# Kernel optimization log

Measured on AMD Instinct MI355X. Metric: run time of the kernel, lower is better.

## Reference

```python
import jax, jax.numpy as jnp
import numpy as np


def setup_inputs() -> dict:
    key = jax.random.key(0)
    k1, k2 = jax.random.split(key)
    B, K, S = 262144, 32, 30
    sparse_code = jax.random.normal(k1, (B, K), dtype=jnp.float32)
    dictionary = jax.random.normal(k2, (S * S, K), dtype=jnp.float32)
    return {"sparse_code": sparse_code, "dictionary": dictionary, "image_size": S}


def reference(sparse_code, dictionary, image_size):
    # matmul(dictionary, sparse_code.T).T == sparse_code @ dictionary.T -> [B, S*S]
    samples = jnp.einsum("bk,dk->bd", sparse_code, dictionary)
    B = samples.shape[0]
    img = samples.reshape(B, image_size, image_size)
    # Serpentine unrolling: flip every odd row (rows 1,3,...,image_size-1)
    img = img.at[:, 1::2, :].set(img[:, 1::2, ::-1])
    return img[:, None, :, :]  # [B, 1, S, S]
```

## Files before the change

### kernel.cpp

```cpp
#include <hip/hip_runtime.h>
#include <hip/hip_bf16.h>


typedef __attribute__((ext_vector_type(8))) short bf16x8;
typedef __attribute__((ext_vector_type(4))) float f32x4;

constexpr int KD    = 32;
constexpr int DDIM  = 900;
constexpr int SDIM  = 30;
constexpr int NCHT  = 57;
constexpr int TROWS = 16;
constexpr int TILES = 8;
constexpr int RPB   = TROWS * TILES;

__device__ __forceinline__ int serp_src(int d) {
    int r = d / SDIM, c = d - r * SDIM;
    return (r & 1) ? (r * SDIM + (SDIM - 1 - c)) : d;
}

__device__ __forceinline__ short f2bf(float x) {
    __hip_bfloat16 h = __float2bfloat16(x);
    short u; __builtin_memcpy(&u, &h, 2); return u;
}

__device__ __forceinline__ void barrier_lds() {
    __builtin_amdgcn_sched_barrier(0);
    asm volatile("s_waitcnt lgkmcnt(0)" ::: "memory");
    __builtin_amdgcn_sched_barrier(0);
    __builtin_amdgcn_s_barrier();
    __builtin_amdgcn_sched_barrier(0);
}

__global__ __launch_bounds__(256) void mfma_decode(
    const float* __restrict__ sc,
    const float* __restrict__ dict,
    float* __restrict__ out,
    int B)
{
    __shared__ alignas(16) float stg[TROWS * DDIM];

    const int t    = threadIdx.x;
    const int lane = t & 63;
    const int wid  = t >> 6;

    bf16x8 df[15];
    #pragma unroll
    for (int j = 0; j < 15; ++j) {
        int ch = wid + 4 * j; if (ch > NCHT - 1) ch = NCHT - 1;
        int d  = ch * 16 + (lane & 15);
        int dd = (d < DDIM) ? d : (DDIM - 1);
        const float* p = dict + (size_t)serp_src(dd) * KD + ((lane >> 4) << 3);
        const float4 f0 = *reinterpret_cast<const float4*>(p);
        const float4 f1 = *reinterpret_cast<const float4*>(p + 4);
        bf16x8 a;
        a[0] = f2bf(f0.x); a[1] = f2bf(f0.y); a[2] = f2bf(f0.z); a[3] = f2bf(f0.w);
        a[4] = f2bf(f1.x); a[5] = f2bf(f1.y); a[6] = f2bf(f1.z); a[7] = f2bf(f1.w);
        df[j] = a;
    }

    const int brow = lane & 15;
    const int k0   = (lane >> 4) << 3;
    const int dloc = (lane >> 4) << 2;
    const long long b0 = (long long)blockIdx.x * RPB;

    const float* ap0 = sc + (size_t)(b0 + brow) * KD + k0;
    float4 pf0 = *reinterpret_cast<const float4*>(ap0);
    float4 pf1 = *reinterpret_cast<const float4*>(ap0 + 4);

    for (int tile = 0; tile < TILES; ++tile) {
        const long long rowg = b0 + (long long)tile * TROWS;

        bf16x8 bb;
        bb[0] = f2bf(pf0.x); bb[1] = f2bf(pf0.y); bb[2] = f2bf(pf0.z); bb[3] = f2bf(pf0.w);
        bb[4] = f2bf(pf1.x); bb[5] = f2bf(pf1.y); bb[6] = f2bf(pf1.z); bb[7] = f2bf(pf1.w);

        if (tile + 1 < TILES) {
            const float* apn = sc + (size_t)(rowg + TROWS + brow) * KD + k0;
            pf0 = *reinterpret_cast<const float4*>(apn);
            pf1 = *reinterpret_cast<const float4*>(apn + 4);
        }

        #pragma unroll
        for (int j = 0; j < 15; ++j) {
            const int ch = wid + 4 * j;
            if (ch < NCHT) {
                f32x4 z = {0.f, 0.f, 0.f, 0.f};
                f32x4 acc = __builtin_amdgcn_mfma_f32_16x16x32_bf16(df[j], bb, z, 0, 0, 0);
                if (ch != 56) {
                    *reinterpret_cast<f32x4*>(&stg[brow * DDIM + ch * 16 + dloc]) = acc;
                } else if (dloc == 0) {
                    *reinterpret_cast<f32x4*>(&stg[brow * DDIM + 896]) = acc;
                }
            }
        }
        barrier_lds();

        float* __restrict__ tbase = out + (size_t)rowg * DDIM;
        const int base = t * 4;
        #pragma unroll
        for (int i = 0; i < 14; ++i) {
            const int o = i * 1024 + base;
            f32x4 v = *reinterpret_cast<const f32x4*>(&stg[o]);
            *reinterpret_cast<f32x4*>(tbase + o) = v;
        }
        if (t < 16) {
            const int o = 14336 + base;
            f32x4 v = *reinterpret_cast<const f32x4*>(&stg[o]);
            *reinterpret_cast<f32x4*>(tbase + o) = v;
        }
        barrier_lds();
    }
}

extern "C" void kernel_launch(void* const* d_in, const int* in_sizes, int n_in,
                              void* d_out, int out_size, void* d_ws, size_t ws_size,
                              hipStream_t stream) {
    const float* sc   = (const float*)d_in[0];
    const float* dict = (const float*)d_in[1];
    float* out        = (float*)d_out;

    const int B = in_sizes[0] / KD;

    mfma_decode<<<dim3((unsigned)(B / RPB)), 256, 0, stream>>>(sc, dict, out, B);
}
```

Before: 203.3 us.

## Double-buffer LDS staging and raise tiles per block to overlap MFMA with stores

Doubles the LDS staging buffer so the MFMA results for the next tile are written into one buffer while the current tile is copied from the other buffer to global memory. This removes one of the two barriers per tile. It also doubles the tiles per block, which halves the grid size and amortizes the dictionary fragment load. The cost is twice the LDS per block (about 115 KB), which limits each CU to one resident block and may reduce latency hiding. The loads of sparse codes are prefetched two tiles ahead.

```diff
diff --git a/kernel.cpp b/kernel.cpp
--- a/kernel.cpp
+++ b/kernel.cpp
@@ -10,8 +10,9 @@
 constexpr int SDIM  = 30;
 constexpr int NCHT  = 57;
 constexpr int TROWS = 16;
-constexpr int TILES = 8;
+constexpr int TILES = 16;
 constexpr int RPB   = TROWS * TILES;
+constexpr int TFL   = TROWS * DDIM;
 
 __device__ __forceinline__ int serp_src(int d) {
     int r = d / SDIM, c = d - r * SDIM;
@@ -37,7 +38,7 @@
     float* __restrict__ out,
     int B)
 {
-    __shared__ alignas(16) float stg[TROWS * DDIM];
+    __shared__ alignas(16) float stg[2][TFL];
 
     const int t    = threadIdx.x;
     const int lane = t & 63;
@@ -63,52 +64,67 @@
     const int dloc = (lane >> 4) << 2;
     const long long b0 = (long long)blockIdx.x * RPB;
 
-    const float* ap0 = sc + (size_t)(b0 + brow) * KD + k0;
-    float4 pf0 = *reinterpret_cast<const float4*>(ap0);
-    float4 pf1 = *reinterpret_cast<const float4*>(ap0 + 4);
-
-    for (int tile = 0; tile < TILES; ++tile) {
-        const long long rowg = b0 + (long long)tile * TROWS;
-
-        bf16x8 bb;
-        bb[0] = f2bf(pf0.x); bb[1] = f2bf(pf0.y); bb[2] = f2bf(pf0.z); bb[3] = f2bf(pf0.w);
-        bb[4] = f2bf(pf1.x); bb[5] = f2bf(pf1.y); bb[6] = f2bf(pf1.z); bb[7] = f2bf(pf1.w);
-
-        if (tile + 1 < TILES) {
-            const float* apn = sc + (size_t)(rowg + TROWS + brow) * KD + k0;
-            pf0 = *reinterpret_cast<const float4*>(apn);
-            pf1 = *reinterpret_cast<const float4*>(apn + 4);
-        }
-
+    auto compute = [&](const bf16x8& bbx, float* buf) {
         #pragma unroll
         for (int j = 0; j < 15; ++j) {
             const int ch = wid + 4 * j;
             if (ch < NCHT) {
                 f32x4 z = {0.f, 0.f, 0.f, 0.f};
-                f32x4 acc = __builtin_amdgcn_mfma_f32_16x16x32_bf16(df[j], bb, z, 0, 0, 0);
+                f32x4 acc = __builtin_amdgcn_mfma_f32_16x16x32_bf16(df[j], bbx, z, 0, 0, 0);
                 if (ch != 56) {
-                    *reinterpret_cast<f32x4*>(&stg[brow * DDIM + ch * 16 + dloc]) = acc;
+                    *reinterpret_cast<f32x4*>(&buf[brow * DDIM + ch * 16 + dloc]) = acc;
                 } else if (dloc == 0) {
-                    *reinterpret_cast<f32x4*>(&stg[brow * DDIM + 896]) = acc;
+                    *reinterpret_cast<f32x4*>(&buf[brow * DDIM + 896]) = acc;
                 }
             }
         }
-        barrier_lds();
+    };
 
-        float* __restrict__ tbase = out + (size_t)rowg * DDIM;
-        const int base = t * 4;
+    auto sc_load = [&](int tt, float4& a, float4& b) {
+        const float* ap = sc + (size_t)(b0 + tt * TROWS + brow) * KD + k0;
+        a = *reinterpret_cast<const float4*>(ap);
+        b = *reinterpret_cast<const float4*>(ap + 4);
+    };
+    auto sc_cvt = [&](const float4& a, const float4& b) {
+        bf16x8 r;
+        r[0] = f2bf(a.x); r[1] = f2bf(a.y); r[2] = f2bf(a.z); r[3] = f2bf(a.w);
+        r[4] = f2bf(b.x); r[5] = f2bf(b.y); r[6] = f2bf(b.z); r[7] = f2bf(b.w);
+        return r;
+    };
+
+    float4 pf0, pf1;
+    sc_load(0, pf0, pf1);
+    bf16x8 bb0 = sc_cvt(pf0, pf1);
+    sc_load(1, pf0, pf1);
+    compute(bb0, stg[0]);
+    barrier_lds();
+
+    int cur = 0;
+    const int base = t * 4;
+
+    for (int tile = 0; tile < TILES; ++tile) {
+        if (tile + 1 < TILES) {
+            bf16x8 nb = sc_cvt(pf0, pf1);
+            if (tile + 2 < TILES) sc_load(tile + 2, pf0, pf1);
+            compute(nb, stg[cur ^ 1]);
+        }
+
+        float* __restrict__ tbase = out + (size_t)(b0 + (long long)tile * TROWS) * DDIM;
+        const float* __restrict__ buf = stg[cur];
         #pragma unroll
         for (int i = 0; i < 14; ++i) {
             const int o = i * 1024 + base;
-            f32x4 v = *reinterpret_cast<const f32x4*>(&stg[o]);
+            f32x4 v = *reinterpret_cast<const f32x4*>(&buf[o]);
             *reinterpret_cast<f32x4*>(tbase + o) = v;
         }
         if (t < 16) {
             const int o = 14336 + base;
-            f32x4 v = *reinterpret_cast<const f32x4*>(&stg[o]);
+            f32x4 v = *reinterpret_cast<const f32x4*>(&buf[o]);
             *reinterpret_cast<f32x4*>(tbase + o) = v;
         }
+
         barrier_lds();
+        cur ^= 1;
     }
 }
 
```

After: 201.9 us. About the same (-0.7%).
